# Kernel optimization log

Measured on AMD Instinct MI355X. Metric: run time of the kernel, lower is better.

The kernel has to match this reference:

```python
import jax, jax.numpy as jnp
import numpy as np

MANT_BITS = 8  # static quantize_param_dict values for Positional_0/1/2
_PWL_X = jnp.linspace(-4.0, 4.0, 33, dtype=jnp.float32)
_PWL_Y = 0.5 * _PWL_X * (1.0 + jax.lax.erf(_PWL_X / jnp.sqrt(jnp.float32(2.0))))


def float2fix(x, mantissa_bits):
    """Fixed-point quantization: round to multiples of 2^-mantissa_bits (STE grad)."""
    s = jnp.float32(2.0 ** mantissa_bits)
    q = jnp.round(x * s) / s
    return x + jax.lax.stop_gradient(q - x)


def pwlin_gelu_basic(x, mantissa_bits_in, mantissa_bits_out):
    """Piecewise-linear GELU: quantized input, linear interp of exact GELU on
    [-4,4] (33 breakpoints), 0 for x<-4, identity for x>4, quantized output."""
    xq = float2fix(x, mantissa_bits_in)
    y = jnp.interp(xq, _PWL_X, _PWL_Y)
    y = jnp.where(xq > 4.0, xq, jnp.where(xq < -4.0, jnp.float32(0.0), y))
    return float2fix(y, mantissa_bits_out)


def setup_inputs() -> dict:
    key = jax.random.key(0)
    k_x, k_w1, k_b1, k_w2, k_b2 = jax.random.split(key, 5)
    dim, ff_dim = 1024, 4096
    B, S = 32, 512
    sc1 = 1.0 / np.sqrt(dim)
    sc2 = 1.0 / np.sqrt(ff_dim)
    return {
        "x": jax.random.normal(k_x, (B, S, dim), dtype=jnp.float32),
        "w1": jax.random.uniform(k_w1, (dim, ff_dim), jnp.float32, -sc1, sc1),
        "b1": jax.random.uniform(k_b1, (ff_dim,), jnp.float32, -sc1, sc1),
        "w2": jax.random.uniform(k_w2, (ff_dim, dim), jnp.float32, -sc2, sc2),
        "b2": jax.random.uniform(k_b2, (dim,), jnp.float32, -sc2, sc2),
    }


def reference(x, w1, b1, w2, b2):
    # fc1 GEMM + quantize epilogue
    h = jnp.einsum("bsd,df->bsf", x, w1) + b1          # [B,S,ff_dim]
    h = float2fix(h, MANT_BITS)                         # Positional_0
    # piecewise-linear GELU with quantized in/out
    h = pwlin_gelu_basic(h, MANT_BITS, MANT_BITS)
    h = float2fix(h, MANT_BITS)                         # Positional_1
    # fc2 GEMM + quantize epilogue
    out = jnp.einsum("bsf,fd->bsd", h, w2) + b2         # [B,S,dim]
    return float2fix(out, MANT_BITS)                    # Positional_2
```

## Files before the change

kernel.cpp:

```cpp
#include <hip/hip_runtime.h>
#include <hip/hip_bf16.h>

typedef __bf16 bf16_t;
typedef __bf16 bf16x8 __attribute__((ext_vector_type(8)));
typedef __bf16 bf16x4 __attribute__((ext_vector_type(4)));
typedef float f32x4 __attribute__((ext_vector_type(4)));

#define QS   256.0f
#define QINV 0.00390625f

__device__ __forceinline__ void async_copy16(const bf16_t* g, bf16_t* l) {
  __builtin_amdgcn_global_load_lds(
      (__attribute__((address_space(1))) void*)g,
      (__attribute__((address_space(3))) void*)l,
      16, 0, 0);
}

template <int SHIFT>
__device__ __forceinline__ void stage_unit(const bf16_t* __restrict__ gk, bf16_t* lbuf,
                                           int K, int halfOff, int tid) {
  const int scb = (((tid & 7) ^ ((tid >> 3) & 7)) << 3);
  const int MASK = (1 << SHIFT) - 1;
#pragma unroll
  for (int q = 0; q < 2; ++q) {
    const int u  = q * 64 + (tid >> 3);
    const int u0 = q * 64 + ((tid >> 6) << 3);
    const int row  = halfOff + (u  & MASK) + ((u  >> SHIFT) << (SHIFT + 1));
    const int row0 = halfOff + (u0 & MASK) + ((u0 >> SHIFT) << (SHIFT + 1));
    async_copy16(gk + (size_t)row * K + scb, lbuf + row0 * 64);
  }
}

__device__ __forceinline__ bf16x8 ldfrag(const bf16_t* buf, int row, int ks, int lq) {
  const int phys = ((ks << 2) | lq) ^ (row & 7);
  return *(const bf16x8*)(buf + row * 64 + (phys << 3));
}

__device__ __forceinline__ void ktile(
    const bf16_t* __restrict__ Ab, const bf16_t* __restrict__ Bb,
    bf16_t* __restrict__ An, bf16_t* __restrict__ Bn,
    const bf16_t* __restrict__ aN, const bf16_t* __restrict__ bN,
    const bool nl, const int tid, const int rA0, const int rB0, const int lq,
    const int K, f32x4 (&acc)[8][4]) {
  bf16x8 fa[2][4];
  bf16x8 fb[2][2][2];

#pragma unroll
  for (int ks = 0; ks < 2; ++ks) {
#pragma unroll
    for (int i = 0; i < 4; ++i) fa[ks][i] = ldfrag(Ab, rA0 + i * 16, ks, lq);
#pragma unroll
    for (int j = 0; j < 2; ++j) fb[0][ks][j] = ldfrag(Bb, rB0 + j * 16, ks, lq);
  }
  if (nl) {
    stage_unit<6>(aN, An, K, 0, tid);
    asm volatile("s_waitcnt vmcnt(4)" ::: "memory");
  } else {
    asm volatile("s_waitcnt vmcnt(2)" ::: "memory");
  }
  __builtin_amdgcn_s_barrier();
  asm volatile("s_waitcnt lgkmcnt(0)" ::: "memory");
  __builtin_amdgcn_sched_barrier(0);
  __builtin_amdgcn_s_setprio(1);
#pragma unroll
  for (int ks = 0; ks < 2; ++ks)
#pragma unroll
    for (int i = 0; i < 4; ++i)
#pragma unroll
      for (int j = 0; j < 2; ++j)
        acc[i][j] = __builtin_amdgcn_mfma_f32_16x16x32_bf16(fa[ks][i], fb[0][ks][j], acc[i][j], 0, 0, 0);
  __builtin_amdgcn_s_setprio(0);
  __builtin_amdgcn_s_barrier();

#pragma unroll
  for (int ks = 0; ks < 2; ++ks)
#pragma unroll
    for (int j = 0; j < 2; ++j) fb[1][ks][j] = ldfrag(Bb, rB0 + 32 + j * 16, ks, lq);
  if (nl) {
    stage_unit<5>(bN, Bn, K, 0, tid);
    asm volatile("s_waitcnt vmcnt(4)" ::: "memory");
  } else {
    asm volatile("s_waitcnt vmcnt(0)" ::: "memory");
  }
  __builtin_amdgcn_s_barrier();
  asm volatile("s_waitcnt lgkmcnt(0)" ::: "memory");
  __builtin_amdgcn_sched_barrier(0);
  __builtin_amdgcn_s_setprio(1);
#pragma unroll
  for (int ks = 0; ks < 2; ++ks)
#pragma unroll
    for (int i = 0; i < 4; ++i)
#pragma unroll
      for (int j = 0; j < 2; ++j)
        acc[i][2 + j] = __builtin_amdgcn_mfma_f32_16x16x32_bf16(fa[ks][i], fb[1][ks][j], acc[i][2 + j], 0, 0, 0);
  __builtin_amdgcn_s_setprio(0);
  __builtin_amdgcn_s_barrier();

#pragma unroll
  for (int ks = 0; ks < 2; ++ks)
#pragma unroll
    for (int i = 0; i < 4; ++i) fa[ks][i] = ldfrag(Ab, rA0 + 64 + i * 16, ks, lq);
  if (nl) stage_unit<5>(bN, Bn, K, 32, tid);
  __builtin_amdgcn_s_barrier();
  asm volatile("s_waitcnt lgkmcnt(0)" ::: "memory");
  __builtin_amdgcn_sched_barrier(0);
  __builtin_amdgcn_s_setprio(1);
#pragma unroll
  for (int ks = 0; ks < 2; ++ks)
#pragma unroll
    for (int i = 0; i < 4; ++i)
#pragma unroll
      for (int j = 0; j < 2; ++j)
        acc[4 + i][2 + j] = __builtin_amdgcn_mfma_f32_16x16x32_bf16(fa[ks][i], fb[1][ks][j], acc[4 + i][2 + j], 0, 0, 0);
  __builtin_amdgcn_s_setprio(0);
  __builtin_amdgcn_s_barrier();

  if (nl) {
    stage_unit<6>(aN, An, K, 64, tid);
    asm volatile("s_waitcnt vmcnt(4)" ::: "memory");
  }
  __builtin_amdgcn_s_barrier();
  __builtin_amdgcn_sched_barrier(0);
  __builtin_amdgcn_s_setprio(1);
#pragma unroll
  for (int ks = 0; ks < 2; ++ks)
#pragma unroll
    for (int i = 0; i < 4; ++i)
#pragma unroll
      for (int j = 0; j < 2; ++j)
        acc[4 + i][j] = __builtin_amdgcn_mfma_f32_16x16x32_bf16(fa[ks][i], fb[0][ks][j], acc[4 + i][j], 0, 0, 0);
  __builtin_amdgcn_s_setprio(0);
  __builtin_amdgcn_s_barrier();
}

template <bool GELU, typename OutT, bool XSWZ>
__global__ __launch_bounds__(512, 2)
void gemm_tile(const bf16_t* __restrict__ A, const bf16_t* __restrict__ Bt,
               const float* __restrict__ bias, OutT* __restrict__ C,
               int M, int N, int K) {
  __shared__ __attribute__((aligned(16))) bf16_t As0[256 * 64];
  __shared__ __attribute__((aligned(16))) bf16_t Bs0[256 * 64];
  __shared__ __attribute__((aligned(16))) bf16_t As1[256 * 64];
  __shared__ __attribute__((aligned(16))) bf16_t Bs1[256 * 64];

  const int tid = threadIdx.x;
  const int lane = tid & 63;
  const int wid = tid >> 6;
  const int wr = wid >> 2;
  const int wc = wid & 3;
  const int l15 = lane & 15;
  const int lq = lane >> 4;

  float ytA = 0.f, ytS = 0.f;
  if (GELU) {
    float xv = -4.0f + 0.25f * (float)lane;
    float y0 = 0.5f * xv * (1.0f + erff(xv * 0.70710678f));
    float xv1 = xv + 0.25f;
    float y1 = 0.5f * xv1 * (1.0f + erff(xv1 * 0.70710678f));
    ytA = y0;
    ytS = y1 - y0;
  }

  int bx = blockIdx.x, by = blockIdx.y;
  if (XSWZ) {
    const int gx = gridDim.x;
    const int nwg = gx * gridDim.y;
    const int f = by * gx + bx;
    const int chunk = nwg >> 3;
    const int f2 = (f & 7) * chunk + (f >> 3);
    bx = f2 % gx;
    by = f2 / gx;
  }

  const int mBase = by * 256;
  const int nBase = bx * 256;
  const bf16_t* aTile = A + (size_t)mBase * K;
  const bf16_t* bTile = Bt + (size_t)nBase * K;

  f32x4 acc[8][4];
#pragma unroll
  for (int i = 0; i < 8; ++i)
#pragma unroll
    for (int j = 0; j < 4; ++j)
      acc[i][j] = (f32x4){0.f, 0.f, 0.f, 0.f};

  const int nT = K >> 6;
  const int rA0 = wr * 128 + l15;
  const int rB0 = wc * 64 + l15;

  stage_unit<6>(aTile, As0, K, 0, tid);
  stage_unit<5>(bTile, Bs0, K, 0, tid);
  stage_unit<5>(bTile, Bs0, K, 32, tid);
  stage_unit<6>(aTile, As0, K, 64, tid);
  asm volatile("s_waitcnt vmcnt(4)" ::: "memory");
  __builtin_amdgcn_s_barrier();

  for (int tt = 0; tt < nT; tt += 2) {
    ktile(As0, Bs0, As1, Bs1,
          aTile + (size_t)(tt + 1) * 64, bTile + (size_t)(tt + 1) * 64,
          true, tid, rA0, rB0, lq, K, acc);
    ktile(As1, Bs1, As0, Bs0,
          aTile + (size_t)(tt + 2) * 64, bTile + (size_t)(tt + 2) * 64,
          (tt + 2 < nT), tid, rA0, rB0, lq, K, acc);
  }

  float bj[4];
#pragma unroll
  for (int j = 0; j < 4; ++j)
    bj[j] = bias[nBase + wc * 64 + j * 16 + l15];

#pragma unroll
  for (int i = 0; i < 8; ++i) {
    const int rb = mBase + wr * 128 + i * 16 + lq * 4;
#pragma unroll
    for (int j = 0; j < 4; ++j) {
      const int cn = nBase + wc * 64 + j * 16 + l15;
#pragma unroll
      for (int r = 0; r < 4; ++r) {
        float c = acc[i][j][r] + bj[j];
        float v;
        if (GELU) {
          float xq = rintf(c * QS) * QINV;
          float t = (xq + 4.0f) * 4.0f;
          int ii = (int)t;
          ii = ii < 0 ? 0 : (ii > 31 ? 31 : ii);
          float f = t - (float)ii;
          float y0 = __shfl(ytA, ii);
          float sl = __shfl(ytS, ii);
          v = fmaf(f, sl, y0);
          v = (xq > 4.0f) ? xq : v;
          v = (xq < -4.0f) ? 0.0f : v;
          v = rintf(v * QS) * QINV;
        } else {
          v = rintf(c * QS) * QINV;
        }
        C[(size_t)(rb + r) * N + cn] = (OutT)v;
      }
    }
  }
}

__global__ void cvt_bf16_kernel(const float* __restrict__ in, bf16_t* __restrict__ out, int n4) {
  int idx = blockIdx.x * blockDim.x + threadIdx.x;
  if (idx < n4) {
    const float4 v = ((const float4*)in)[idx];
    bf16x4 o;
    o[0] = (bf16_t)v.x; o[1] = (bf16_t)v.y; o[2] = (bf16_t)v.z; o[3] = (bf16_t)v.w;
    ((bf16x4*)out)[idx] = o;
  }
}

__global__ void transpose_cvt_kernel(const float* __restrict__ in, bf16_t* __restrict__ out,
                                     int R, int C) {
  __shared__ float t[32][33];
  const int c0 = blockIdx.x * 32;
  const int r0 = blockIdx.y * 32;
  const int tx = threadIdx.x;
  const int ty = threadIdx.y;
#pragma unroll
  for (int dy = 0; dy < 32; dy += 8)
    t[ty + dy][tx] = in[(size_t)(r0 + ty + dy) * C + c0 + tx];
  __syncthreads();
#pragma unroll
  for (int dy = 0; dy < 32; dy += 8)
    out[(size_t)(c0 + ty + dy) * R + r0 + tx] = (bf16_t)t[tx][ty + dy];
}

extern "C" void kernel_launch(void* const* d_in, const int* in_sizes, int n_in,
                              void* d_out, int out_size, void* d_ws, size_t ws_size,
                              hipStream_t stream) {
  const float* x  = (const float*)d_in[0];
  const float* w1 = (const float*)d_in[1];
  const float* b1 = (const float*)d_in[2];
  const float* w2 = (const float*)d_in[3];
  const float* b2 = (const float*)d_in[4];
  float* out = (float*)d_out;

  const int M = 16384, D = 1024, F = 4096;

  char* ws = (char*)d_ws;
  size_t off = 0;
  bf16_t* xb  = (bf16_t*)(ws + off); off += (size_t)M * D * 2;
  bf16_t* w1t = (bf16_t*)(ws + off); off += (size_t)D * F * 2;
  bf16_t* w2t = (bf16_t*)(ws + off); off += (size_t)F * D * 2;
  bf16_t* h   = (bf16_t*)(ws + off);

  cvt_bf16_kernel<<<(M * D / 4 + 255) / 256, 256, 0, stream>>>(x, xb, M * D / 4);
  transpose_cvt_kernel<<<dim3(F / 32, D / 32), dim3(32, 8), 0, stream>>>(w1, w1t, D, F);
  transpose_cvt_kernel<<<dim3(D / 32, F / 32), dim3(32, 8), 0, stream>>>(w2, w2t, F, D);

  gemm_tile<true, bf16_t, false><<<dim3(F / 256, M / 256), 512, 0, stream>>>(xb, w1t, b1, h, M, F, D);
  gemm_tile<false, float, true><<<dim3(D / 256, M / 256), 512, 0, stream>>>(h, w2t, b2, out, M, D, F);
}
```

Before: 417.1 us.

## Use simple 128x128 GEMM for fc1, merge prep kernels, drop sched barriers

Replaces the fc1 GEMM with a new, simpler 128x128-tile kernel that is single-buffered and synchronises with __syncthreads on every K step. It also fuses the three convert/transpose launches into one prep kernel, removes the XCD grid swizzle from the fc2 GEMM, and deletes the sched_barrier hints in the pipelined 256-tile kernel. Together these aim to cut launch overhead and change occupancy. The cost is losing the hand-tuned double-buffered pipeline for fc1, the L2 locality from the swizzle, and explicit scheduling control.

```diff
diff --git a/kernel.cpp b/kernel.cpp
--- a/kernel.cpp
+++ b/kernel.cpp
@@ -14,6 +14,112 @@
       (__attribute__((address_space(1))) void*)g,
       (__attribute__((address_space(3))) void*)l,
       16, 0, 0);
+}
+
+__device__ __forceinline__ float gelu_quant(float c, float ytA, float ytS) {
+  float xq = rintf(c * QS) * QINV;
+  float t = (xq + 4.0f) * 4.0f;
+  int ii = (int)t;
+  ii = ii < 0 ? 0 : (ii > 31 ? 31 : ii);
+  float f = t - (float)ii;
+  float y0 = __shfl(ytA, ii);
+  float sl = __shfl(ytS, ii);
+  float v = fmaf(f, sl, y0);
+  v = (xq > 4.0f) ? xq : v;
+  v = (xq < -4.0f) ? 0.0f : v;
+  return rintf(v * QS) * QINV;
+}
+
+template <bool GELU, typename OutT>
+__global__ __launch_bounds__(256, 4)
+void gemm128(const bf16_t* __restrict__ A, const bf16_t* __restrict__ Bt,
+             const float* __restrict__ bias, OutT* __restrict__ C,
+             int M, int N, int K) {
+  __shared__ __attribute__((aligned(16))) bf16_t As[128 * 64];
+  __shared__ __attribute__((aligned(16))) bf16_t Bs[128 * 64];
+
+  const int tid = threadIdx.x;
+  const int lane = tid & 63;
+  const int wv = tid >> 6;
+  const int wy = wv >> 1;
+  const int wx = wv & 1;
+  const int l15 = lane & 15;
+  const int lq = lane >> 4;
+
+  float ytA = 0.f, ytS = 0.f;
+  if (GELU) {
+    float xv = -4.0f + 0.25f * (float)lane;
+    float y0 = 0.5f * xv * (1.0f + erff(xv * 0.70710678f));
+    float xv1 = xv + 0.25f;
+    float y1 = 0.5f * xv1 * (1.0f + erff(xv1 * 0.70710678f));
+    ytA = y0;
+    ytS = y1 - y0;
+  }
+
+  const int mBase = blockIdx.y * 128;
+  const int nBase = blockIdx.x * 128;
+  const bf16_t* aTile = A + (size_t)mBase * K;
+  const bf16_t* bTile = Bt + (size_t)nBase * K;
+
+  f32x4 acc[4][4];
+#pragma unroll
+  for (int i = 0; i < 4; ++i)
+#pragma unroll
+    for (int j = 0; j < 4; ++j)
+      acc[i][j] = (f32x4){0.f, 0.f, 0.f, 0.f};
+
+  const int srow = tid >> 3;
+  const int scb = (((tid & 7) ^ ((tid >> 3) & 7)) * 8);
+  const int swz_r = l15 & 7;
+
+  for (int k0 = 0; k0 < K; k0 += 64) {
+#pragma unroll
+    for (int p = 0; p < 4; ++p) {
+      const int row = p * 32 + srow;
+      const size_t go = (size_t)row * K + k0 + scb;
+      const int lo = (p * 256 + wv * 64) * 8;
+      async_copy16(aTile + go, As + lo);
+      async_copy16(bTile + go, Bs + lo);
+    }
+    __syncthreads();
+
+#pragma unroll
+    for (int ks = 0; ks < 2; ++ks) {
+      const int swzA = ((ks * 4 + lq) ^ swz_r) * 8;
+      bf16x8 af[4], bfr[4];
+#pragma unroll
+      for (int i = 0; i < 4; ++i) {
+        af[i]  = *(const bf16x8*)(As + (wy * 64 + i * 16 + l15) * 64 + swzA);
+        bfr[i] = *(const bf16x8*)(Bs + (wx * 64 + i * 16 + l15) * 64 + swzA);
+      }
+#pragma unroll
+      for (int i = 0; i < 4; ++i)
+#pragma unroll
+        for (int j = 0; j < 4; ++j)
+          acc[i][j] = __builtin_amdgcn_mfma_f32_16x16x32_bf16(af[i], bfr[j], acc[i][j], 0, 0, 0);
+    }
+    __syncthreads();
+  }
+
+  float bj[4];
+#pragma unroll
+  for (int j = 0; j < 4; ++j)
+    bj[j] = bias[nBase + wx * 64 + j * 16 + l15];
+
+#pragma unroll
+  for (int i = 0; i < 4; ++i) {
+    const int rb = mBase + wy * 64 + i * 16 + lq * 4;
+#pragma unroll
+    for (int j = 0; j < 4; ++j) {
+      const int cn = nBase + wx * 64 + j * 16 + l15;
+#pragma unroll
+      for (int r = 0; r < 4; ++r) {
+        float c = acc[i][j][r] + bj[j];
+        float v = GELU ? gelu_quant(c, ytA, ytS) : rintf(c * QS) * QINV;
+        C[(size_t)(rb + r) * N + cn] = (OutT)v;
+      }
+    }
+  }
 }
 
 template <int SHIFT>
@@ -60,7 +166,6 @@
   }
   __builtin_amdgcn_s_barrier();
   asm volatile("s_waitcnt lgkmcnt(0)" ::: "memory");
-  __builtin_amdgcn_sched_barrier(0);
   __builtin_amdgcn_s_setprio(1);
 #pragma unroll
   for (int ks = 0; ks < 2; ++ks)
@@ -84,7 +189,6 @@
   }
   __builtin_amdgcn_s_barrier();
   asm volatile("s_waitcnt lgkmcnt(0)" ::: "memory");
-  __builtin_amdgcn_sched_barrier(0);
   __builtin_amdgcn_s_setprio(1);
 #pragma unroll
   for (int ks = 0; ks < 2; ++ks)
@@ -103,7 +207,6 @@
   if (nl) stage_unit<5>(bN, Bn, K, 32, tid);
   __builtin_amdgcn_s_barrier();
   asm volatile("s_waitcnt lgkmcnt(0)" ::: "memory");
-  __builtin_amdgcn_sched_barrier(0);
   __builtin_amdgcn_s_setprio(1);
 #pragma unroll
   for (int ks = 0; ks < 2; ++ks)
@@ -120,7 +223,6 @@
     asm volatile("s_waitcnt vmcnt(4)" ::: "memory");
   }
   __builtin_amdgcn_s_barrier();
-  __builtin_amdgcn_sched_barrier(0);
   __builtin_amdgcn_s_setprio(1);
 #pragma unroll
   for (int ks = 0; ks < 2; ++ks)
@@ -133,11 +235,11 @@
   __builtin_amdgcn_s_barrier();
 }
 
-template <bool GELU, typename OutT, bool XSWZ>
+template <bool GELU, typename OutT>
 __global__ __launch_bounds__(512, 2)
-void gemm_tile(const bf16_t* __restrict__ A, const bf16_t* __restrict__ Bt,
-               const float* __restrict__ bias, OutT* __restrict__ C,
-               int M, int N, int K) {
+void gemm256(const bf16_t* __restrict__ A, const bf16_t* __restrict__ Bt,
+             const float* __restrict__ bias, OutT* __restrict__ C,
+             int M, int N, int K) {
   __shared__ __attribute__((aligned(16))) bf16_t As0[256 * 64];
   __shared__ __attribute__((aligned(16))) bf16_t Bs0[256 * 64];
   __shared__ __attribute__((aligned(16))) bf16_t As1[256 * 64];
@@ -161,19 +263,8 @@
     ytS = y1 - y0;
   }
 
-  int bx = blockIdx.x, by = blockIdx.y;
-  if (XSWZ) {
-    const int gx = gridDim.x;
-    const int nwg = gx * gridDim.y;
-    const int f = by * gx + bx;
-    const int chunk = nwg >> 3;
-    const int f2 = (f & 7) * chunk + (f >> 3);
-    bx = f2 % gx;
-    by = f2 / gx;
-  }
-
-  const int mBase = by * 256;
-  const int nBase = bx * 256;
+  const int mBase = blockIdx.y * 256;
+  const int nBase = blockIdx.x * 256;
   const bf16_t* aTile = A + (size_t)mBase * K;
   const bf16_t* bTile = Bt + (size_t)nBase * K;
 
@@ -218,52 +309,49 @@
 #pragma unroll
       for (int r = 0; r < 4; ++r) {
         float c = acc[i][j][r] + bj[j];
-        float v;
-        if (GELU) {
-          float xq = rintf(c * QS) * QINV;
-          float t = (xq + 4.0f) * 4.0f;
-          int ii = (int)t;
-          ii = ii < 0 ? 0 : (ii > 31 ? 31 : ii);
-          float f = t - (float)ii;
-          float y0 = __shfl(ytA, ii);
-          float sl = __shfl(ytS, ii);
-          v = fmaf(f, sl, y0);
-          v = (xq > 4.0f) ? xq : v;
-          v = (xq < -4.0f) ? 0.0f : v;
-          v = rintf(v * QS) * QINV;
-        } else {
-          v = rintf(c * QS) * QINV;
-        }
+        float v = GELU ? gelu_quant(c, ytA, ytS) : rintf(c * QS) * QINV;
         C[(size_t)(rb + r) * N + cn] = (OutT)v;
       }
     }
   }
 }
 
-__global__ void cvt_bf16_kernel(const float* __restrict__ in, bf16_t* __restrict__ out, int n4) {
-  int idx = blockIdx.x * blockDim.x + threadIdx.x;
-  if (idx < n4) {
-    const float4 v = ((const float4*)in)[idx];
+__global__ __launch_bounds__(256)
+void prep_kernel(const float* __restrict__ x, bf16_t* __restrict__ xb,
+                 const float* __restrict__ w1, bf16_t* __restrict__ w1t,
+                 const float* __restrict__ w2, bf16_t* __restrict__ w2t) {
+  __shared__ float t[32][33];
+  const int id = blockIdx.x;
+  const int tid = threadIdx.x;
+  if (id < 16384) {
+    const int idx = id * 256 + tid;
+    const float4 v = ((const float4*)x)[idx];
     bf16x4 o;
     o[0] = (bf16_t)v.x; o[1] = (bf16_t)v.y; o[2] = (bf16_t)v.z; o[3] = (bf16_t)v.w;
-    ((bf16x4*)out)[idx] = o;
-  }
-}
-
-__global__ void transpose_cvt_kernel(const float* __restrict__ in, bf16_t* __restrict__ out,
-                                     int R, int C) {
-  __shared__ float t[32][33];
-  const int c0 = blockIdx.x * 32;
-  const int r0 = blockIdx.y * 32;
-  const int tx = threadIdx.x;
-  const int ty = threadIdx.y;
-#pragma unroll
-  for (int dy = 0; dy < 32; dy += 8)
-    t[ty + dy][tx] = in[(size_t)(r0 + ty + dy) * C + c0 + tx];
-  __syncthreads();
-#pragma unroll
-  for (int dy = 0; dy < 32; dy += 8)
-    out[(size_t)(c0 + ty + dy) * R + r0 + tx] = (bf16_t)t[tx][ty + dy];
+    ((bf16x4*)xb)[idx] = o;
+  } else {
+    const float* in; bf16_t* out; int R, C, bx, by;
+    if (id < 20480) {
+      const int id2 = id - 16384;
+      in = w1; out = w1t; R = 1024; C = 4096;
+      bx = id2 & 127; by = id2 >> 7;
+    } else {
+      const int id3 = id - 20480;
+      in = w2; out = w2t; R = 4096; C = 1024;
+      bx = id3 & 31; by = id3 >> 5;
+    }
+    const int c0 = bx * 32;
+    const int r0 = by * 32;
+    const int tx = tid & 31;
+    const int ty = tid >> 5;
+#pragma unroll
+    for (int dy = 0; dy < 32; dy += 8)
+      t[ty + dy][tx] = in[(size_t)(r0 + ty + dy) * C + c0 + tx];
+    __syncthreads();
+#pragma unroll
+    for (int dy = 0; dy < 32; dy += 8)
+      out[(size_t)(c0 + ty + dy) * R + r0 + tx] = (bf16_t)t[tx][ty + dy];
+  }
 }
 
 extern "C" void kernel_launch(void* const* d_in, const int* in_sizes, int n_in,
@@ -285,10 +373,8 @@
   bf16_t* w2t = (bf16_t*)(ws + off); off += (size_t)F * D * 2;
   bf16_t* h   = (bf16_t*)(ws + off);
 
-  cvt_bf16_kernel<<<(M * D / 4 + 255) / 256, 256, 0, stream>>>(x, xb, M * D / 4);
-  transpose_cvt_kernel<<<dim3(F / 32, D / 32), dim3(32, 8), 0, stream>>>(w1, w1t, D, F);
-  transpose_cvt_kernel<<<dim3(D / 32, F / 32), dim3(32, 8), 0, stream>>>(w2, w2t, F, D);
-
-  gemm_tile<true, bf16_t, false><<<dim3(F / 256, M / 256), 512, 0, stream>>>(xb, w1t, b1, h, M, F, D);
-  gemm_tile<false, float, true><<<dim3(D / 256, M / 256), 512, 0, stream>>>(h, w2t, b2, out, M, D, F);
-}
+  prep_kernel<<<16384 + 4096 + 4096, 256, 0, stream>>>(x, xb, w1, w1t, w2, w2t);
+
+  gemm128<true, bf16_t><<<dim3(F / 128, M / 128), 256, 0, stream>>>(xb, w1t, b1, h, M, F, D);
+  gemm256<false, float><<<dim3(D / 256, M / 256), 512, 0, stream>>>(h, w2t, b2, out, M, D, F);
+}
```

After: 429.9 us. +3.0%, slower.
